# Kernel tuning notes

Measured on AMD Instinct MI355X. Metric: run time of the kernel, lower is better.

The kernel has to match this reference:

```python
import jax, jax.numpy as jnp
import numpy as np

N, E, D_IN, D_OUT = 50000, 800000, 128, 128
LN_EPS = 1e-5


def setup_inputs() -> dict:
    key = jax.random.key(0)
    ks = jax.random.split(key, 7)
    x = jax.random.normal(ks[0], (N, D_IN), dtype=jnp.float32)
    adj = jax.random.randint(ks[1], (2, E), 0, N, dtype=jnp.int32)  # edge_index
    scale = 1.0 / np.sqrt(D_IN)
    W_gcn = jax.random.normal(ks[2], (D_IN, D_OUT), dtype=jnp.float32) * scale
    b_gcn = jax.random.normal(ks[3], (D_OUT,), dtype=jnp.float32) * 0.02
    W_lin = jax.random.normal(ks[4], (D_IN, D_OUT), dtype=jnp.float32) * scale
    ln_w = jnp.ones((D_OUT,), dtype=jnp.float32)
    ln_b = jnp.zeros((D_OUT,), dtype=jnp.float32)
    return {"adj": adj, "x": x, "W_gcn": W_gcn, "b_gcn": b_gcn,
            "W_lin": W_lin, "ln_w": ln_w, "ln_b": ln_b}


def _gcn_conv(x, edge_index, W, b):
    """PyG GCNConv: add self-loops, symmetric D^-1/2 (A+I) D^-1/2 normalization."""
    n = x.shape[0]
    loop = jnp.arange(n, dtype=edge_index.dtype)
    src = jnp.concatenate([edge_index[0], loop])  # message sources (x_j)
    dst = jnp.concatenate([edge_index[1], loop])  # aggregation targets
    ones = jnp.ones(src.shape[0], dtype=x.dtype)
    deg = jax.ops.segment_sum(ones, dst, num_segments=n)
    dinv = jnp.where(deg > 0, jax.lax.rsqrt(deg), 0.0)
    norm = dinv[src] * dinv[dst]                   # [E+N]
    h = x @ W                                      # [N, D_OUT] project first (PyG order)
    msg = h[src] * norm[:, None]                   # gather + scale
    agg = jax.ops.segment_sum(msg, dst, num_segments=n)
    return agg + b


def _layer_norm(y, w, b):
    mu = jnp.mean(y, axis=-1, keepdims=True)
    var = jnp.mean(jnp.square(y - mu), axis=-1, keepdims=True)
    return (y - mu) * jax.lax.rsqrt(var + LN_EPS) * w + b


def reference(adj, x, W_gcn, b_gcn, W_lin, ln_w, ln_b):
    x1 = _gcn_conv(x, adj, W_gcn, b_gcn)
    x2 = x @ W_lin                                  # bias=False linear
    return _layer_norm(x1 + x2 + 1e-6, ln_w, ln_b)
```

## Files before the change

kernel.cpp:

```cpp
#include <hip/hip_runtime.h>
#include <hip/hip_bf16.h>

#define NN 50000
#define EE 800000
#define DD 128
#define CB 196
#define NFB 1563
#define EBLK 4096
#define NEB 196

typedef __attribute__((ext_vector_type(8))) short bf16x8;
typedef __attribute__((ext_vector_type(4))) float f32x4;

static __device__ __forceinline__ unsigned short f2bf(float f) {
  union { float f; unsigned u; } v; v.f = f;
  unsigned r = v.u + 0x7FFFu + ((v.u >> 16) & 1u);
  return (unsigned short)(r >> 16);
}
static __device__ __forceinline__ float bf2f(unsigned short h) {
  union { unsigned u; float f; } v; v.u = ((unsigned)h) << 16;
  return v.f;
}

__global__ __launch_bounds__(256) void k_p0(
    const int* __restrict__ dst, int* __restrict__ coarseCnt,
    const float* __restrict__ Wg, const float* __restrict__ Wl,
    unsigned short* __restrict__ Wt, const float4* __restrict__ x4,
    ushort4* __restrict__ xb4) {
  int b = blockIdx.x, t = threadIdx.x;
  if (b < NEB) {
    __shared__ int cnt[CB];
    for (int i = t; i < CB; i += 256) cnt[i] = 0;
    __syncthreads();
    int e0 = b * EBLK;
    for (int i = t; i < EBLK; i += 256) {
      int e = e0 + i;
      if (e < EE) atomicAdd(&cnt[dst[e] >> 8], 1);
    }
    __syncthreads();
    for (int i = t; i < CB; i += 256)
      if (cnt[i]) atomicAdd(&coarseCnt[i], cnt[i]);
  } else if (b < NEB + 32) {
    for (int i = (b - NEB) * 256 + t; i < DD * 256; i += 32 * 256) {
      int n = i >> 8, k = i & 255;
      float v = (k < 128) ? Wg[k * DD + n] : Wl[(k - 128) * DD + n];
      Wt[i] = f2bf(v);
    }
  } else {
    int base = (b - NEB - 32) * 1024 + t;
#pragma unroll
    for (int k = 0; k < 4; k++) {
      int i = base + k * 256;
      if (i < NN * 32) {
        float4 v = x4[i];
        ushort4 o;
        o.x = f2bf(v.x); o.y = f2bf(v.y); o.z = f2bf(v.z); o.w = f2bf(v.w);
        xb4[i] = o;
      }
    }
  }
}

__global__ __launch_bounds__(512) void k_p1a(const int* __restrict__ src,
                                             const int* __restrict__ dst,
                                             const int* __restrict__ coarseCnt,
                                             int* __restrict__ cursor0,
                                             unsigned int* __restrict__ pairs) {
  __shared__ unsigned int stage[EBLK];
  __shared__ int sc[256];
  __shared__ int cnt[CB], rb[CB], cur[CB];
  int t = threadIdx.x;
  int e0 = blockIdx.x * EBLK;
  int own = 0;
  if (t < CB) { cnt[t] = 0; cur[t] = 0; }
  if (t < 256) { own = (t < CB) ? coarseCnt[t] : 0; sc[t] = own; }
  __syncthreads();
  for (int i = t; i < EBLK; i += 512) {
    int e = e0 + i;
    unsigned int p = 0xFFFFFFFFu;
    if (e < EE) {
      int d = dst[e], s = src[e];
      int cb = d >> 8;
      p = (unsigned int)s | ((unsigned int)(d & 255) << 16) | ((unsigned int)cb << 24);
      atomicAdd(&cnt[cb], 1);
    }
    stage[i] = p;
  }
  for (int off = 1; off < 256; off <<= 1) {
    __syncthreads();
    int tmp = (t < 256 && t >= off) ? sc[t - off] : 0;
    __syncthreads();
    if (t < 256 && t >= off) sc[t] += tmp;
  }
  __syncthreads();
  if (t < CB) {
    int excl = sc[t] - own;
    rb[t] = excl + (cnt[t] ? atomicAdd(&cursor0[t], cnt[t]) : 0);
  }
  __syncthreads();
  for (int i = t; i < EBLK; i += 512) {
    unsigned int p = stage[i];
    if (p != 0xFFFFFFFFu) {
      int cb = p >> 24;
      int ofs = atomicAdd(&cur[cb], 1);
      pairs[rb[cb] + ofs] = p;
    }
  }
}

__global__ __launch_bounds__(512) void k_p1b(
    const unsigned int* __restrict__ pairs, const int* __restrict__ coarseCnt,
    const unsigned short* __restrict__ xb,
    int* __restrict__ deg, float* __restrict__ dinv, int* __restrict__ rowStart,
    unsigned short* __restrict__ srcU16, unsigned short* __restrict__ xs) {
  __shared__ int ldeg[256], lscan[256], lcur[256];
  __shared__ float ldinvs[256];
  __shared__ int wsum[8];
  int b = blockIdx.x, t = threadIdx.x;
  int n0 = b << 8;
  int nloc = NN - n0; if (nloc > 256) nloc = 256;
  int partial = 0;
  for (int i = t; i < b; i += 512) partial += coarseCnt[i];
#pragma unroll
  for (int off = 32; off > 0; off >>= 1) partial += __shfl_xor(partial, off);
  if ((t & 63) == 0) wsum[t >> 6] = partial;
  if (t < 256) ldeg[t] = 0;
  __syncthreads();
  int start = wsum[0] + wsum[1] + wsum[2] + wsum[3] +
              wsum[4] + wsum[5] + wsum[6] + wsum[7];
  int cnt = coarseCnt[b];
  for (int i = t; i < cnt; i += 512)
    atomicAdd(&ldeg[(pairs[start + i] >> 16) & 255], 1);
  __syncthreads();
  int dg = (t < 256) ? ldeg[t] : 0;
  if (t < 256) lscan[t] = dg;
  for (int off = 1; off < 256; off <<= 1) {
    __syncthreads();
    int tmp = (t < 256 && t >= off) ? lscan[t - off] : 0;
    __syncthreads();
    if (t < 256 && t >= off) lscan[t] += tmp;
  }
  __syncthreads();
  if (t < 256) {
    int rs = start + lscan[t] - dg;
    lcur[t] = rs;
    float di = rsqrtf((float)(dg + 1));
    ldinvs[t] = di;
    if (t < nloc) { deg[n0 + t] = dg; dinv[n0 + t] = di; rowStart[n0 + t] = rs; }
  }
  __syncthreads();
  for (int i = t; i < cnt; i += 512) {
    unsigned int pr = pairs[start + i];
    int pos = atomicAdd(&lcur[(pr >> 16) & 255], 1);
    srcU16[pos] = (unsigned short)(pr & 0xFFFFu);
  }
  for (int i = t; i < nloc * 16; i += 512) {
    int rr = i >> 4, q = i & 15;
    bf16x8 v = *(const bf16x8*)(xb + (size_t)(n0 + rr) * DD + q * 8);
    float di = ldinvs[rr];
    bf16x8 o;
#pragma unroll
    for (int k = 0; k < 8; k++) o[k] = (short)f2bf(bf2f((unsigned short)v[k]) * di);
    *(bf16x8*)(xs + (size_t)(n0 + rr) * DD + q * 8) = o;
  }
}

static __device__ __forceinline__ void gather16(
    const unsigned short* __restrict__ xs, const unsigned short* __restrict__ srcU16,
    int js, int cnt, int r, int srcLaneBase, float* acc) {
  for (int base = 0; base < cnt; base += 16) {
    int idx = (base + r < cnt) ? (int)srcU16[js + base + r] : 0;
    int m = cnt - base; if (m > 16) m = 16;
    int j = 0;
    for (; j + 8 <= m; j += 8) {
      int s0 = __shfl(idx, srcLaneBase + j);
      int s1 = __shfl(idx, srcLaneBase + j + 1);
      int s2 = __shfl(idx, srcLaneBase + j + 2);
      int s3 = __shfl(idx, srcLaneBase + j + 3);
      int s4 = __shfl(idx, srcLaneBase + j + 4);
      int s5 = __shfl(idx, srcLaneBase + j + 5);
      int s6 = __shfl(idx, srcLaneBase + j + 6);
      int s7 = __shfl(idx, srcLaneBase + j + 7);
      bf16x8 v0 = *(const bf16x8*)(xs + (size_t)s0 * DD + r * 8);
      bf16x8 v1 = *(const bf16x8*)(xs + (size_t)s1 * DD + r * 8);
      bf16x8 v2 = *(const bf16x8*)(xs + (size_t)s2 * DD + r * 8);
      bf16x8 v3 = *(const bf16x8*)(xs + (size_t)s3 * DD + r * 8);
      bf16x8 v4 = *(const bf16x8*)(xs + (size_t)s4 * DD + r * 8);
      bf16x8 v5 = *(const bf16x8*)(xs + (size_t)s5 * DD + r * 8);
      bf16x8 v6 = *(const bf16x8*)(xs + (size_t)s6 * DD + r * 8);
      bf16x8 v7 = *(const bf16x8*)(xs + (size_t)s7 * DD + r * 8);
#pragma unroll
      for (int k = 0; k < 8; k++) acc[k] += bf2f((unsigned short)v0[k]);
#pragma unroll
      for (int k = 0; k < 8; k++) acc[k] += bf2f((unsigned short)v1[k]);
#pragma unroll
      for (int k = 0; k < 8; k++) acc[k] += bf2f((unsigned short)v2[k]);
#pragma unroll
      for (int k = 0; k < 8; k++) acc[k] += bf2f((unsigned short)v3[k]);
#pragma unroll
      for (int k = 0; k < 8; k++) acc[k] += bf2f((unsigned short)v4[k]);
#pragma unroll
      for (int k = 0; k < 8; k++) acc[k] += bf2f((unsigned short)v5[k]);
#pragma unroll
      for (int k = 0; k < 8; k++) acc[k] += bf2f((unsigned short)v6[k]);
#pragma unroll
      for (int k = 0; k < 8; k++) acc[k] += bf2f((unsigned short)v7[k]);
    }
    for (; j < m; j++) {
      int s = __shfl(idx, srcLaneBase + j);
      bf16x8 v = *(const bf16x8*)(xs + (size_t)s * DD + r * 8);
#pragma unroll
      for (int k = 0; k < 8; k++) acc[k] += bf2f((unsigned short)v[k]);
    }
  }
}

__global__ __launch_bounds__(512) void k_mega4(
    const unsigned short* __restrict__ xs, const unsigned short* __restrict__ xb,
    const int* __restrict__ rowStart, const int* __restrict__ deg,
    const unsigned short* __restrict__ srcU16, const float* __restrict__ dinv,
    const unsigned short* __restrict__ Wt, const float* __restrict__ bgcn,
    const float* __restrict__ lnw, const float* __restrict__ lnb,
    float* __restrict__ out) {
  __shared__ unsigned short abuf[32 * 136];
  int b = blockIdx.x, t = threadIdx.x;
  int n0 = b * 32;
  int g = t >> 4, r = t & 15;
  int lane = t & 63;
  int srcLaneBase = lane & 48;
  int node = n0 + g;
  bool valid = (node < NN);
  int nc = valid ? node : (NN - 1);
  float acc[8];
  {
    bf16x8 va = *(const bf16x8*)(xs + (size_t)nc * DD + r * 8);
#pragma unroll
    for (int k = 0; k < 8; k++) acc[k] = bf2f((unsigned short)va[k]);
  }
  int js = valid ? rowStart[nc] : 0;
  int cnt = valid ? deg[nc] : 0;
  gather16(xs, srcU16, js, cnt, r, srcLaneBase, acc);
  {
    float d = dinv[nc];
    bf16x8 o;
#pragma unroll
    for (int k = 0; k < 8; k++) o[k] = valid ? (short)f2bf(acc[k] * d) : (short)0;
    *(bf16x8*)&abuf[g * 136 + r * 8] = o;
  }
  __syncthreads();
  if (t < 128) {
    int w = t >> 6, lane2 = t & 63;
    int quad = lane2 >> 4, rr = lane2 & 15;
    int mloc = w * 16 + rr;
    int rowA = n0 + mloc; int rc = (rowA < NN) ? rowA : (NN - 1);
    f32x4 zero = {0.f, 0.f, 0.f, 0.f};
    f32x4 macc[8];
#pragma unroll
    for (int i = 0; i < 8; i++) macc[i] = zero;
#pragma unroll
    for (int ks = 0; ks < 8; ks++) {
      bf16x8 a;
      if (ks < 4) a = *(const bf16x8*)&abuf[mloc * 136 + ks * 32 + quad * 8];
      else        a = *(const bf16x8*)(xb + (size_t)rc * DD + (ks - 4) * 32 + quad * 8);
#pragma unroll
      for (int nt = 0; nt < 8; nt++) {
        bf16x8 bb = *(const bf16x8*)(Wt + (size_t)(nt * 16 + rr) * 256 + ks * 32 + quad * 8);
        macc[nt] = __builtin_amdgcn_mfma_f32_16x16x32_bf16(a, bb, macc[nt], 0, 0, 0);
      }
    }
    float bg[8], lw[8], lb[8];
#pragma unroll
    for (int nt = 0; nt < 8; nt++) {
      int col = nt * 16 + rr;
      bg[nt] = bgcn[col] + 1e-6f;
      lw[nt] = lnw[col];
      lb[nt] = lnb[col];
    }
#pragma unroll
    for (int reg = 0; reg < 4; reg++) {
      float y[8];
      float s1 = 0.f, s2 = 0.f;
#pragma unroll
      for (int nt = 0; nt < 8; nt++) {
        y[nt] = macc[nt][reg] + bg[nt];
        s1 += y[nt];
        s2 += y[nt] * y[nt];
      }
#pragma unroll
      for (int off = 1; off < 16; off <<= 1) {
        s1 += __shfl_xor(s1, off);
        s2 += __shfl_xor(s2, off);
      }
      float mu = s1 * (1.0f / 128.0f);
      float var = s2 * (1.0f / 128.0f) - mu * mu;
      float inv = rsqrtf(var + 1e-5f);
      int row = n0 + w * 16 + quad * 4 + reg;
      if (row < NN) {
#pragma unroll
        for (int nt = 0; nt < 8; nt++) {
          out[(size_t)row * DD + nt * 16 + rr] = (y[nt] - mu) * inv * lw[nt] + lb[nt];
        }
      }
    }
  }
}

extern "C" void kernel_launch(void* const* d_in, const int* in_sizes, int n_in,
                              void* d_out, int out_size, void* d_ws, size_t ws_size,
                              hipStream_t stream) {
  const int* adj = (const int*)d_in[0];
  const float* x = (const float*)d_in[1];
  const float* Wg = (const float*)d_in[2];
  const float* bg = (const float*)d_in[3];
  const float* Wl = (const float*)d_in[4];
  const float* lw = (const float*)d_in[5];
  const float* lb = (const float*)d_in[6];
  const int* srcp = adj;
  const int* dstp = adj + EE;
  float* out = (float*)d_out;

  char* ws = (char*)d_ws;
  size_t off = 0;
  auto alloc = [&](size_t bytes) -> void* {
    void* p = ws + off;
    off += (bytes + 255) & ~(size_t)255;
    return p;
  };
  int* zb = (int*)alloc((size_t)512 * 4);
  int* coarseCnt = zb;
  int* cursor0 = zb + 256;
  unsigned int* pairs = (unsigned int*)alloc((size_t)EE * 4);
  unsigned short* srcU16 = (unsigned short*)alloc((size_t)EE * 2);
  int* deg = (int*)alloc((size_t)NN * 4);
  float* dinv = (float*)alloc((size_t)NN * 4);
  int* rowStart = (int*)alloc((size_t)NN * 4);
  unsigned short* xb = (unsigned short*)alloc((size_t)NN * DD * 2);
  unsigned short* xs = (unsigned short*)alloc((size_t)NN * DD * 2);
  unsigned short* Wt = (unsigned short*)alloc((size_t)DD * 256 * 2);
  (void)ws_size; (void)in_sizes; (void)n_in; (void)out_size;

  hipMemsetAsync(zb, 0, (size_t)512 * 4, stream);
  k_p0<<<NEB + 32 + 1563, 256, 0, stream>>>(dstp, coarseCnt, Wg, Wl, Wt,
                                            (const float4*)x, (ushort4*)xb);
  k_p1a<<<NEB, 512, 0, stream>>>(srcp, dstp, coarseCnt, cursor0, pairs);
  k_p1b<<<CB, 512, 0, stream>>>(pairs, coarseCnt, xb, deg, dinv, rowStart,
                                srcU16, xs);
  k_mega4<<<NFB, 512, 0, stream>>>(xs, xb, rowStart, deg, srcU16, dinv, Wt,
                                   bg, lw, lb, out);
}
```

Measured before the change: 182.2 us.

## Replace two-pass coarse-bucket CSR build with global degree atomics and direct fill

Builds CSR by counting per-node degree with global atomics in the first kernel, scanning per 256-node block, then scattering source indices directly via per-node cursor atomics. This removes the intermediate pairs buffer and its two-level bucket sort. The x scaling work moves into a separate fully parallel grid. It adds 800k global atomics twice, with scattered, poorly coalesced writes. The memset now relies on deg being allocated directly after zb.

Result: slower. 240.2 us (+31.8%).

```diff
diff --git a/kernel.cpp b/kernel.cpp
--- a/kernel.cpp
+++ b/kernel.cpp
@@ -8,6 +8,8 @@
 #define NFB 1563
 #define EBLK 4096
 #define NEB 196
+#define XSB 3125
+#define SCB 391
 
 typedef __attribute__((ext_vector_type(8))) short bf16x8;
 typedef __attribute__((ext_vector_type(4))) float f32x4;
@@ -24,6 +26,7 @@
 
 __global__ __launch_bounds__(256) void k_p0(
     const int* __restrict__ dst, int* __restrict__ coarseCnt,
+    int* __restrict__ deg,
     const float* __restrict__ Wg, const float* __restrict__ Wl,
     unsigned short* __restrict__ Wt, const float4* __restrict__ x4,
     ushort4* __restrict__ xb4) {
@@ -35,7 +38,11 @@
     int e0 = b * EBLK;
     for (int i = t; i < EBLK; i += 256) {
       int e = e0 + i;
-      if (e < EE) atomicAdd(&cnt[dst[e] >> 8], 1);
+      if (e < EE) {
+        int d = dst[e];
+        atomicAdd(&cnt[d >> 8], 1);
+        atomicAdd(&deg[d], 1);
+      }
     }
     __syncthreads();
     for (int i = t; i < CB; i += 256)
@@ -61,107 +68,64 @@
   }
 }
 
-__global__ __launch_bounds__(512) void k_p1a(const int* __restrict__ src,
-                                             const int* __restrict__ dst,
-                                             const int* __restrict__ coarseCnt,
-                                             int* __restrict__ cursor0,
-                                             unsigned int* __restrict__ pairs) {
-  __shared__ unsigned int stage[EBLK];
-  __shared__ int sc[256];
-  __shared__ int cnt[CB], rb[CB], cur[CB];
-  int t = threadIdx.x;
-  int e0 = blockIdx.x * EBLK;
-  int own = 0;
-  if (t < CB) { cnt[t] = 0; cur[t] = 0; }
-  if (t < 256) { own = (t < CB) ? coarseCnt[t] : 0; sc[t] = own; }
-  __syncthreads();
-  for (int i = t; i < EBLK; i += 512) {
-    int e = e0 + i;
-    unsigned int p = 0xFFFFFFFFu;
-    if (e < EE) {
-      int d = dst[e], s = src[e];
-      int cb = d >> 8;
-      p = (unsigned int)s | ((unsigned int)(d & 255) << 16) | ((unsigned int)cb << 24);
-      atomicAdd(&cnt[cb], 1);
-    }
-    stage[i] = p;
-  }
+__global__ __launch_bounds__(256) void k_scan(
+    const int* __restrict__ coarseCnt, const int* __restrict__ deg,
+    int* __restrict__ rowStart, int* __restrict__ cursor,
+    float* __restrict__ dinv) {
+  __shared__ int lscan[256];
+  __shared__ int wsum[4];
+  int b = blockIdx.x, t = threadIdx.x;
+  int n0 = b << 8;
+  int partial = 0;
+  for (int i = t; i < b; i += 256) partial += coarseCnt[i];
+#pragma unroll
+  for (int off = 32; off > 0; off >>= 1) partial += __shfl_xor(partial, off);
+  if ((t & 63) == 0) wsum[t >> 6] = partial;
+  int n = n0 + t;
+  int dg = (n < NN) ? deg[n] : 0;
+  lscan[t] = dg;
   for (int off = 1; off < 256; off <<= 1) {
     __syncthreads();
-    int tmp = (t < 256 && t >= off) ? sc[t - off] : 0;
+    int tmp = (t >= off) ? lscan[t - off] : 0;
     __syncthreads();
-    if (t < 256 && t >= off) sc[t] += tmp;
+    if (t >= off) lscan[t] += tmp;
   }
   __syncthreads();
-  if (t < CB) {
-    int excl = sc[t] - own;
-    rb[t] = excl + (cnt[t] ? atomicAdd(&cursor0[t], cnt[t]) : 0);
-  }
-  __syncthreads();
-  for (int i = t; i < EBLK; i += 512) {
-    unsigned int p = stage[i];
-    if (p != 0xFFFFFFFFu) {
-      int cb = p >> 24;
-      int ofs = atomicAdd(&cur[cb], 1);
-      pairs[rb[cb] + ofs] = p;
-    }
-  }
-}
-
-__global__ __launch_bounds__(512) void k_p1b(
-    const unsigned int* __restrict__ pairs, const int* __restrict__ coarseCnt,
-    const unsigned short* __restrict__ xb,
-    int* __restrict__ deg, float* __restrict__ dinv, int* __restrict__ rowStart,
-    unsigned short* __restrict__ srcU16, unsigned short* __restrict__ xs) {
-  __shared__ int ldeg[256], lscan[256], lcur[256];
-  __shared__ float ldinvs[256];
-  __shared__ int wsum[8];
+  int start = wsum[0] + wsum[1] + wsum[2] + wsum[3];
+  if (n < NN) {
+    int rs = start + lscan[t] - dg;
+    rowStart[n] = rs;
+    cursor[n] = rs;
+    dinv[n] = rsqrtf((float)(dg + 1));
+  }
+}
+
+__global__ __launch_bounds__(256) void k_fill(
+    const int* __restrict__ src, const int* __restrict__ dst,
+    int* __restrict__ cursor, const unsigned short* __restrict__ xb,
+    const float* __restrict__ dinv, unsigned short* __restrict__ xs,
+    unsigned short* __restrict__ srcU16) {
   int b = blockIdx.x, t = threadIdx.x;
-  int n0 = b << 8;
-  int nloc = NN - n0; if (nloc > 256) nloc = 256;
-  int partial = 0;
-  for (int i = t; i < b; i += 512) partial += coarseCnt[i];
-#pragma unroll
-  for (int off = 32; off > 0; off >>= 1) partial += __shfl_xor(partial, off);
-  if ((t & 63) == 0) wsum[t >> 6] = partial;
-  if (t < 256) ldeg[t] = 0;
-  __syncthreads();
-  int start = wsum[0] + wsum[1] + wsum[2] + wsum[3] +
-              wsum[4] + wsum[5] + wsum[6] + wsum[7];
-  int cnt = coarseCnt[b];
-  for (int i = t; i < cnt; i += 512)
-    atomicAdd(&ldeg[(pairs[start + i] >> 16) & 255], 1);
-  __syncthreads();
-  int dg = (t < 256) ? ldeg[t] : 0;
-  if (t < 256) lscan[t] = dg;
-  for (int off = 1; off < 256; off <<= 1) {
-    __syncthreads();
-    int tmp = (t < 256 && t >= off) ? lscan[t - off] : 0;
-    __syncthreads();
-    if (t < 256 && t >= off) lscan[t] += tmp;
-  }
-  __syncthreads();
-  if (t < 256) {
-    int rs = start + lscan[t] - dg;
-    lcur[t] = rs;
-    float di = rsqrtf((float)(dg + 1));
-    ldinvs[t] = di;
-    if (t < nloc) { deg[n0 + t] = dg; dinv[n0 + t] = di; rowStart[n0 + t] = rs; }
-  }
-  __syncthreads();
-  for (int i = t; i < cnt; i += 512) {
-    unsigned int pr = pairs[start + i];
-    int pos = atomicAdd(&lcur[(pr >> 16) & 255], 1);
-    srcU16[pos] = (unsigned short)(pr & 0xFFFFu);
-  }
-  for (int i = t; i < nloc * 16; i += 512) {
-    int rr = i >> 4, q = i & 15;
-    bf16x8 v = *(const bf16x8*)(xb + (size_t)(n0 + rr) * DD + q * 8);
-    float di = ldinvs[rr];
+  if (b < XSB) {
+    int i = b * 256 + t;
+    int row = i >> 4;
+    float di = dinv[row];
+    bf16x8 v = *(const bf16x8*)(xb + (size_t)i * 8);
     bf16x8 o;
 #pragma unroll
     for (int k = 0; k < 8; k++) o[k] = (short)f2bf(bf2f((unsigned short)v[k]) * di);
-    *(bf16x8*)(xs + (size_t)(n0 + rr) * DD + q * 8) = o;
+    *(bf16x8*)(xs + (size_t)i * 8) = o;
+  } else {
+    int e0 = (b - XSB) * 2048 + t;
+#pragma unroll
+    for (int k = 0; k < 8; k++) {
+      int e = e0 + k * 256;
+      if (e < EE) {
+        int d = dst[e];
+        int pos = atomicAdd(&cursor[d], 1);
+        srcU16[pos] = (unsigned short)src[e];
+      }
+    }
   }
 }
 
@@ -328,23 +292,21 @@
   };
   int* zb = (int*)alloc((size_t)512 * 4);
   int* coarseCnt = zb;
-  int* cursor0 = zb + 256;
-  unsigned int* pairs = (unsigned int*)alloc((size_t)EE * 4);
-  unsigned short* srcU16 = (unsigned short*)alloc((size_t)EE * 2);
   int* deg = (int*)alloc((size_t)NN * 4);
   float* dinv = (float*)alloc((size_t)NN * 4);
   int* rowStart = (int*)alloc((size_t)NN * 4);
+  int* cursor = (int*)alloc((size_t)NN * 4);
+  unsigned short* srcU16 = (unsigned short*)alloc((size_t)EE * 2);
   unsigned short* xb = (unsigned short*)alloc((size_t)NN * DD * 2);
   unsigned short* xs = (unsigned short*)alloc((size_t)NN * DD * 2);
   unsigned short* Wt = (unsigned short*)alloc((size_t)DD * 256 * 2);
   (void)ws_size; (void)in_sizes; (void)n_in; (void)out_size;
 
-  hipMemsetAsync(zb, 0, (size_t)512 * 4, stream);
-  k_p0<<<NEB + 32 + 1563, 256, 0, stream>>>(dstp, coarseCnt, Wg, Wl, Wt,
+  hipMemsetAsync(zb, 0, (size_t)512 * 4 + (size_t)NN * 4, stream);
+  k_p0<<<NEB + 32 + 1563, 256, 0, stream>>>(dstp, coarseCnt, deg, Wg, Wl, Wt,
                                             (const float4*)x, (ushort4*)xb);
-  k_p1a<<<NEB, 512, 0, stream>>>(srcp, dstp, coarseCnt, cursor0, pairs);
-  k_p1b<<<CB, 512, 0, stream>>>(pairs, coarseCnt, xb, deg, dinv, rowStart,
-                                srcU16, xs);
+  k_scan<<<CB, 256, 0, stream>>>(coarseCnt, deg, rowStart, cursor, dinv);
+  k_fill<<<XSB + SCB, 256, 0, stream>>>(srcp, dstp, cursor, xb, dinv, xs, srcU16);
   k_mega4<<<NFB, 512, 0, stream>>>(xs, xb, rowStart, deg, srcU16, dinv, Wt,
                                    bg, lw, lb, out);
 }
```

## Replace atomic coarse-bucket cursors with per-block histogram prefix and local sort

Applied to the files above, without the earlier changes.

The edge bucketing pass now writes a per-block coarse histogram instead of doing global atomics. The scatter kernel prefix-sums these histograms to get deterministic offsets, sorts each 2048-edge chunk in LDS, and writes contiguous runs to global memory, which drops the memset and the global cursor atomics. The per-node CSR fill stages source indices in LDS before a coalesced write-out, and the dinv-scaling of x moves into a separate elementwise kernel. In exchange, every scatter block serially reads the full 391x196 histogram, and the extra launch adds overhead.

New measurement: 200.1 us. 9.9% more time.

```diff
diff --git a/kernel.cpp b/kernel.cpp
--- a/kernel.cpp
+++ b/kernel.cpp
@@ -6,8 +6,10 @@
 #define DD 128
 #define CB 196
 #define NFB 1563
-#define EBLK 4096
-#define NEB 196
+#define EBLK 2048
+#define NEBK 391
+#define XSB 3125
+#define SSZ 5120
 
 typedef __attribute__((ext_vector_type(8))) short bf16x8;
 typedef __attribute__((ext_vector_type(4))) float f32x4;
@@ -23,12 +25,12 @@
 }
 
 __global__ __launch_bounds__(256) void k_p0(
-    const int* __restrict__ dst, int* __restrict__ coarseCnt,
+    const int* __restrict__ dst, int* __restrict__ hist,
     const float* __restrict__ Wg, const float* __restrict__ Wl,
     unsigned short* __restrict__ Wt, const float4* __restrict__ x4,
     ushort4* __restrict__ xb4) {
   int b = blockIdx.x, t = threadIdx.x;
-  if (b < NEB) {
+  if (b < NEBK) {
     __shared__ int cnt[CB];
     for (int i = t; i < CB; i += 256) cnt[i] = 0;
     __syncthreads();
@@ -38,16 +40,15 @@
       if (e < EE) atomicAdd(&cnt[dst[e] >> 8], 1);
     }
     __syncthreads();
-    for (int i = t; i < CB; i += 256)
-      if (cnt[i]) atomicAdd(&coarseCnt[i], cnt[i]);
-  } else if (b < NEB + 32) {
-    for (int i = (b - NEB) * 256 + t; i < DD * 256; i += 32 * 256) {
+    for (int i = t; i < CB; i += 256) hist[b * CB + i] = cnt[i];
+  } else if (b < NEBK + 32) {
+    for (int i = (b - NEBK) * 256 + t; i < DD * 256; i += 32 * 256) {
       int n = i >> 8, k = i & 255;
       float v = (k < 128) ? Wg[k * DD + n] : Wl[(k - 128) * DD + n];
       Wt[i] = f2bf(v);
     }
   } else {
-    int base = (b - NEB - 32) * 1024 + t;
+    int base = (b - NEBK - 32) * 1024 + t;
 #pragma unroll
     for (int k = 0; k < 4; k++) {
       int i = base + k * 256;
@@ -61,31 +62,35 @@
   }
 }
 
-__global__ __launch_bounds__(512) void k_p1a(const int* __restrict__ src,
-                                             const int* __restrict__ dst,
-                                             const int* __restrict__ coarseCnt,
-                                             int* __restrict__ cursor0,
-                                             unsigned int* __restrict__ pairs) {
-  __shared__ unsigned int stage[EBLK];
+__global__ __launch_bounds__(512) void k_scatter(
+    const int* __restrict__ src, const int* __restrict__ dst,
+    const int* __restrict__ hist, int* __restrict__ coarseTot,
+    unsigned int* __restrict__ pairs) {
+  __shared__ unsigned int rec[EBLK];
+  __shared__ unsigned int sorted[EBLK];
+  __shared__ int tot[CB], chunk[CB], own[CB], cur[CB], gofs[CB];
   __shared__ int sc[256];
-  __shared__ int cnt[CB], rb[CB], cur[CB];
-  int t = threadIdx.x;
-  int e0 = blockIdx.x * EBLK;
-  int own = 0;
-  if (t < CB) { cnt[t] = 0; cur[t] = 0; }
-  if (t < 256) { own = (t < CB) ? coarseCnt[t] : 0; sc[t] = own; }
-  __syncthreads();
-  for (int i = t; i < EBLK; i += 512) {
-    int e = e0 + i;
-    unsigned int p = 0xFFFFFFFFu;
-    if (e < EE) {
-      int d = dst[e], s = src[e];
-      int cb = d >> 8;
-      p = (unsigned int)s | ((unsigned int)(d & 255) << 16) | ((unsigned int)cb << 24);
-      atomicAdd(&cnt[cb], 1);
-    }
-    stage[i] = p;
-  }
+  int blk = blockIdx.x, t = threadIdx.x;
+  int e0 = blk * EBLK;
+  int vcnt = EE - e0; if (vcnt > EBLK) vcnt = EBLK;
+  for (int i = t; i < vcnt; i += 512) {
+    int d = dst[e0 + i], s = src[e0 + i];
+    rec[i] = (unsigned int)s | ((unsigned int)(d & 255) << 16) |
+             ((unsigned int)(d >> 8) << 24);
+  }
+  if (t < CB) {
+    int to = 0, ch = 0, ow = 0;
+    for (int b2 = 0; b2 < NEBK; ++b2) {
+      int v = hist[b2 * CB + t];
+      to += v;
+      ch += (b2 < blk) ? v : 0;
+      ow = (b2 == blk) ? v : ow;
+    }
+    tot[t] = to; chunk[t] = ch; own[t] = ow;
+    if (blk == 0) coarseTot[t] = to;
+  }
+  __syncthreads();
+  if (t < 256) sc[t] = (t < CB) ? tot[t] : 0;
   for (int off = 1; off < 256; off <<= 1) {
     __syncthreads();
     int tmp = (t < 256 && t >= off) ? sc[t - off] : 0;
@@ -93,34 +98,47 @@
     if (t < 256 && t >= off) sc[t] += tmp;
   }
   __syncthreads();
+  if (t < CB) gofs[t] = (sc[t] - tot[t]) + chunk[t];
+  __syncthreads();
+  if (t < 256) sc[t] = (t < CB) ? own[t] : 0;
+  for (int off = 1; off < 256; off <<= 1) {
+    __syncthreads();
+    int tmp = (t < 256 && t >= off) ? sc[t - off] : 0;
+    __syncthreads();
+    if (t < 256 && t >= off) sc[t] += tmp;
+  }
+  __syncthreads();
   if (t < CB) {
-    int excl = sc[t] - own;
-    rb[t] = excl + (cnt[t] ? atomicAdd(&cursor0[t], cnt[t]) : 0);
-  }
-  __syncthreads();
-  for (int i = t; i < EBLK; i += 512) {
-    unsigned int p = stage[i];
-    if (p != 0xFFFFFFFFu) {
-      int cb = p >> 24;
-      int ofs = atomicAdd(&cur[cb], 1);
-      pairs[rb[cb] + ofs] = p;
-    }
+    int lo = sc[t] - own[t];
+    cur[t] = lo;
+    gofs[t] -= lo;
+  }
+  __syncthreads();
+  for (int i = t; i < vcnt; i += 512) {
+    unsigned int r = rec[i];
+    int cb = r >> 24;
+    int p = atomicAdd(&cur[cb], 1);
+    sorted[p] = r;
+  }
+  __syncthreads();
+  for (int i = t; i < vcnt; i += 512) {
+    unsigned int r = sorted[i];
+    pairs[gofs[r >> 24] + i] = r;
   }
 }
 
 __global__ __launch_bounds__(512) void k_p1b(
-    const unsigned int* __restrict__ pairs, const int* __restrict__ coarseCnt,
-    const unsigned short* __restrict__ xb,
+    const unsigned int* __restrict__ pairs, const int* __restrict__ coarseTot,
     int* __restrict__ deg, float* __restrict__ dinv, int* __restrict__ rowStart,
-    unsigned short* __restrict__ srcU16, unsigned short* __restrict__ xs) {
+    unsigned short* __restrict__ srcU16) {
   __shared__ int ldeg[256], lscan[256], lcur[256];
-  __shared__ float ldinvs[256];
   __shared__ int wsum[8];
+  __shared__ unsigned short ssrc[SSZ];
   int b = blockIdx.x, t = threadIdx.x;
   int n0 = b << 8;
   int nloc = NN - n0; if (nloc > 256) nloc = 256;
   int partial = 0;
-  for (int i = t; i < b; i += 512) partial += coarseCnt[i];
+  for (int i = t; i < b; i += 512) partial += coarseTot[i];
 #pragma unroll
   for (int off = 32; off > 0; off >>= 1) partial += __shfl_xor(partial, off);
   if ((t & 63) == 0) wsum[t >> 6] = partial;
@@ -128,7 +146,7 @@
   __syncthreads();
   int start = wsum[0] + wsum[1] + wsum[2] + wsum[3] +
               wsum[4] + wsum[5] + wsum[6] + wsum[7];
-  int cnt = coarseCnt[b];
+  int cnt = coarseTot[b];
   for (int i = t; i < cnt; i += 512)
     atomicAdd(&ldeg[(pairs[start + i] >> 16) & 255], 1);
   __syncthreads();
@@ -141,28 +159,41 @@
     if (t < 256 && t >= off) lscan[t] += tmp;
   }
   __syncthreads();
+  bool useStage = (cnt <= SSZ);
   if (t < 256) {
-    int rs = start + lscan[t] - dg;
-    lcur[t] = rs;
-    float di = rsqrtf((float)(dg + 1));
-    ldinvs[t] = di;
-    if (t < nloc) { deg[n0 + t] = dg; dinv[n0 + t] = di; rowStart[n0 + t] = rs; }
+    int lofs = lscan[t] - dg;
+    lcur[t] = lofs;
+    if (t < nloc) {
+      deg[n0 + t] = dg;
+      dinv[n0 + t] = rsqrtf((float)(dg + 1));
+      rowStart[n0 + t] = start + lofs;
+    }
   }
   __syncthreads();
   for (int i = t; i < cnt; i += 512) {
     unsigned int pr = pairs[start + i];
     int pos = atomicAdd(&lcur[(pr >> 16) & 255], 1);
-    srcU16[pos] = (unsigned short)(pr & 0xFFFFu);
-  }
-  for (int i = t; i < nloc * 16; i += 512) {
-    int rr = i >> 4, q = i & 15;
-    bf16x8 v = *(const bf16x8*)(xb + (size_t)(n0 + rr) * DD + q * 8);
-    float di = ldinvs[rr];
-    bf16x8 o;
-#pragma unroll
-    for (int k = 0; k < 8; k++) o[k] = (short)f2bf(bf2f((unsigned short)v[k]) * di);
-    *(bf16x8*)(xs + (size_t)(n0 + rr) * DD + q * 8) = o;
-  }
+    unsigned short v = (unsigned short)(pr & 0xFFFFu);
+    if (useStage) ssrc[pos] = v;
+    else          srcU16[start + pos] = v;
+  }
+  if (useStage) {
+    __syncthreads();
+    for (int i = t; i < cnt; i += 512) srcU16[start + i] = ssrc[i];
+  }
+}
+
+__global__ __launch_bounds__(256) void k_xs(
+    const unsigned short* __restrict__ xb, const float* __restrict__ dinv,
+    unsigned short* __restrict__ xs) {
+  int i = blockIdx.x * 256 + threadIdx.x;
+  int row = i >> 4;
+  float di = dinv[row];
+  bf16x8 v = *(const bf16x8*)(xb + (size_t)i * 8);
+  bf16x8 o;
+#pragma unroll
+  for (int k = 0; k < 8; k++) o[k] = (short)f2bf(bf2f((unsigned short)v[k]) * di);
+  *(bf16x8*)(xs + (size_t)i * 8) = o;
 }
 
 static __device__ __forceinline__ void gather16(
@@ -326,9 +357,8 @@
     off += (bytes + 255) & ~(size_t)255;
     return p;
   };
-  int* zb = (int*)alloc((size_t)512 * 4);
-  int* coarseCnt = zb;
-  int* cursor0 = zb + 256;
+  int* hist = (int*)alloc((size_t)NEBK * CB * 4);
+  int* coarseTot = (int*)alloc((size_t)256 * 4);
   unsigned int* pairs = (unsigned int*)alloc((size_t)EE * 4);
   unsigned short* srcU16 = (unsigned short*)alloc((size_t)EE * 2);
   int* deg = (int*)alloc((size_t)NN * 4);
@@ -339,12 +369,11 @@
   unsigned short* Wt = (unsigned short*)alloc((size_t)DD * 256 * 2);
   (void)ws_size; (void)in_sizes; (void)n_in; (void)out_size;
 
-  hipMemsetAsync(zb, 0, (size_t)512 * 4, stream);
-  k_p0<<<NEB + 32 + 1563, 256, 0, stream>>>(dstp, coarseCnt, Wg, Wl, Wt,
-                                            (const float4*)x, (ushort4*)xb);
-  k_p1a<<<NEB, 512, 0, stream>>>(srcp, dstp, coarseCnt, cursor0, pairs);
-  k_p1b<<<CB, 512, 0, stream>>>(pairs, coarseCnt, xb, deg, dinv, rowStart,
-                                srcU16, xs);
+  k_p0<<<NEBK + 32 + 1563, 256, 0, stream>>>(dstp, hist, Wg, Wl, Wt,
+                                             (const float4*)x, (ushort4*)xb);
+  k_scatter<<<NEBK, 512, 0, stream>>>(srcp, dstp, hist, coarseTot, pairs);
+  k_p1b<<<CB, 512, 0, stream>>>(pairs, coarseTot, deg, dinv, rowStart, srcU16);
+  k_xs<<<XSB, 256, 0, stream>>>(xb, dinv, xs);
   k_mega4<<<NFB, 512, 0, stream>>>(xs, xb, rowStart, deg, srcU16, dinv, Wt,
                                    bg, lw, lb, out);
 }
```
